# Optimization experiments

Hardware: AMD Instinct MI355X
Metric: run time of the kernel (lower is better)

Reference implementation:

```python
import jax, jax.numpy as jnp
import numpy as np

B, T, C, HR = 8, 4096, 256, 4
N_LAYER, LAYER_ID = 12, 3
HID = HR * C


def _fancy_decay_first():
    # Faithful reproduction of VRWKV_SpatialMix._init_weights(init_mode='fancy')
    r01 = LAYER_ID / (N_LAYER - 1)
    h = np.arange(C, dtype=np.float32)
    decay = -5.0 + 8.0 * (h / (C - 1)) ** (0.7 + 1.3 * r01)
    zig = ((np.arange(1, C + 1) % 3) - 1).astype(np.float32) * 0.5
    first = np.float32(np.log(0.3)) + zig
    return jnp.asarray(decay, jnp.float32), jnp.asarray(first, jnp.float32)


def setup_inputs() -> dict:
    key = jax.random.key(0)
    ks = jax.random.split(key, 12)
    s = 0.02  # small weight scale keeps exp(k) well-conditioned
    decay, first = _fancy_decay_first()
    return {
        "x": jax.random.normal(ks[0], (B, T, C), jnp.float32),
        "Wk": jax.random.normal(ks[1], (C, C), jnp.float32) * s,
        "Wv": jax.random.normal(ks[2], (C, C), jnp.float32) * s,
        "Wr": jax.random.normal(ks[3], (C, C), jnp.float32) * s,
        "Wo": jax.random.normal(ks[4], (C, C), jnp.float32) * s,
        "Wk_ffn": jax.random.normal(ks[5], (C, HID), jnp.float32) * s,
        "Wv_ffn": jax.random.normal(ks[6], (HID, C), jnp.float32) * s,
        "Wr_ffn": jax.random.normal(ks[7], (C, C), jnp.float32) * s,
        "g1": 1.0 + 0.1 * jax.random.normal(ks[8], (C,), jnp.float32),
        "b1": 0.1 * jax.random.normal(ks[9], (C,), jnp.float32),
        "g2": 1.0 + 0.1 * jax.random.normal(ks[10], (C,), jnp.float32),
        "b2": 0.1 * jax.random.normal(ks[11], (C,), jnp.float32),
        "spatial_decay": decay,
        "spatial_first": first,
    }


def _ln(x, g, b):
    m = jnp.mean(x, axis=-1, keepdims=True)
    v = jnp.var(x, axis=-1, keepdims=True)
    return (x - m) * jax.lax.rsqrt(v + 1e-5) * g + b


def _wkv(w, u, k, v):
    # Numerically-stable log-space WKV recurrence (same math as wkv_cuda):
    # y_t = (sum_{i<t} e^{w*(t-1-i)+k_i} v_i + e^{u+k_t} v_t)
    #     / (sum_{i<t} e^{w*(t-1-i)+k_i}     + e^{u+k_t})
    # w,u: [C]; k,v: [B,T,C] -> y: [B,T,C]
    Bb, Tt, Cc = k.shape
    kT = jnp.swapaxes(k, 0, 1)  # [T,B,C]
    vT = jnp.swapaxes(v, 0, 1)

    def step(carry, kv):
        p, q, o = carry           # [B,C] num / den / running max exponent
        kt, vt = kv               # [B,C]
        no = jnp.maximum(o, u + kt)
        A = jnp.exp(o - no)
        E = jnp.exp(u + kt - no)
        y = (A * p + E * vt) / (A * q + E)
        no2 = jnp.maximum(w + o, kt)
        A2 = jnp.exp(w + o - no2)
        E2 = jnp.exp(kt - no2)
        return (A2 * p + E2 * vt, A2 * q + E2, no2), y

    init = (jnp.zeros((Bb, Cc), k.dtype),
            jnp.zeros((Bb, Cc), k.dtype),
            jnp.full((Bb, Cc), -1e38, k.dtype))
    _, yT = jax.lax.scan(step, init, (kT, vT))
    return jnp.swapaxes(yT, 0, 1)


def reference(x, Wk, Wv, Wr, Wo, Wk_ffn, Wv_ffn, Wr_ffn, g1, b1, g2, b2,
              spatial_decay, spatial_first):
    Tlen = x.shape[1]
    # --- SpatialMix (shift_pixel=0 -> xk=xv=xr=h, key_norm=False) ---
    h = _ln(x, g1, b1)
    k = h @ Wk
    v = h @ Wv
    sr = jax.nn.sigmoid(h @ Wr)
    y = _wkv(spatial_decay / Tlen, spatial_first / Tlen, k, v)
    x = x + (sr * y) @ Wo
    # --- ChannelMix (square-ReLU MLP, sigmoid receptance gate) ---
    h2 = _ln(x, g2, b2)
    kk = jnp.square(jax.nn.relu(h2 @ Wk_ffn))
    x = x + jax.nn.sigmoid(h2 @ Wr_ffn) * (kk @ Wv_ffn)
    return x
```

## Files before the change

kernel.cpp:

```cpp
#include <hip/hip_runtime.h>
#include <hip/hip_bf16.h>
#include <math.h>

#define TDIM 4096
#define CDIM 256
#define BDIM 8
#define NTOK (BDIM * TDIM)
#define HIDDIM 1024
#define NCHUNK 128
#define CHLEN 32

typedef float f32x4 __attribute__((ext_vector_type(4)));
typedef __bf16 bf16x8 __attribute__((ext_vector_type(8)));
typedef __bf16 bf16x4 __attribute__((ext_vector_type(4)));

#define GLDS16(gp, lp) __builtin_amdgcn_global_load_lds( \
    (const __attribute__((address_space(1))) void*)(gp), \
    (__attribute__((address_space(3))) void*)(lp), 16, 0, 0)

#define WAITCNT_VM6  0x0F76
#define WAITCNT_VM4  0x0F74
#define WAITCNT_VM2  0x0F72
#define WAITCNT_VM0  0x0F70
#define WAITCNT_VM20 0x4F74

__device__ __forceinline__ float sigm(float v) { return 1.0f / (1.0f + __expf(-v)); }

__global__ __launch_bounds__(256) void pack_weights(
    const float* __restrict__ Wk, const float* __restrict__ Wv,
    const float* __restrict__ Wr, const float* __restrict__ Wo,
    const float* __restrict__ Wkf, const float* __restrict__ Wvf,
    const float* __restrict__ Wrf,
    __bf16* __restrict__ WkvrT, __bf16* __restrict__ WoT,
    __bf16* __restrict__ Wkfr, unsigned char* __restrict__ Wvf8) {
  long long j = (long long)blockIdx.x * 256 + threadIdx.x;
  if (j < 196608) {
    int n = (int)(j >> 8), k = (int)(j & 255);
    const float* src = (n < 256) ? Wk : (n < 512 ? Wv : Wr);
    WkvrT[j] = (__bf16)src[k * 256 + (n & 255)];
    return;
  }
  j -= 196608;
  if (j < 65536) { int n = (int)(j >> 8), k = (int)(j & 255);
    WoT[j] = (__bf16)Wo[k * 256 + n]; return; }
  j -= 65536;
  if (j < 327680) { int n = (int)(j >> 8), k = (int)(j & 255);
    Wkfr[j] = (__bf16)(n < 1024 ? Wkf[(long long)k * 1024 + n]
                                : Wrf[k * 256 + (n - 1024)]);
    return; }
  j -= 327680;
  if (j < 65536) {
    const long long d = j * 4;
    const int n = (int)(d >> 10), k0 = (int)(d & 1023);
    int w = 0;
    w = __builtin_amdgcn_cvt_pk_fp8_f32(Wvf[(long long)k0 * 256 + n],
                                        Wvf[(long long)(k0 + 1) * 256 + n], w, false);
    w = __builtin_amdgcn_cvt_pk_fp8_f32(Wvf[(long long)(k0 + 2) * 256 + n],
                                        Wvf[(long long)(k0 + 3) * 256 + n], w, true);
    *(int*)&Wvf8[d] = w;
    return;
  }
}

__global__ __launch_bounds__(256) void ln_kernel(
    const float* __restrict__ x, const float* __restrict__ gamma,
    const float* __restrict__ beta, __bf16* __restrict__ h) {
  const int wave = threadIdx.x >> 6, lane = threadIdx.x & 63;
  const long long row = (long long)blockIdx.x * 4 + wave;
  const long long base = row * CDIM + lane * 4;
  const f32x4 v = *(const f32x4*)&x[base];
  float s = v[0] + v[1] + v[2] + v[3];
  float s2 = v[0]*v[0] + v[1]*v[1] + v[2]*v[2] + v[3]*v[3];
  #pragma unroll
  for (int o = 1; o < 64; o <<= 1) { s += __shfl_xor(s, o); s2 += __shfl_xor(s2, o); }
  const float mean = s * (1.0f / CDIM);
  const float var = s2 * (1.0f / CDIM) - mean * mean;
  const float rstd = rsqrtf(var + 1e-5f);
  const f32x4 g4 = *(const f32x4*)&gamma[lane * 4];
  const f32x4 b4 = *(const f32x4*)&beta[lane * 4];
  bf16x4 o;
  #pragma unroll
  for (int r = 0; r < 4; r++) o[r] = (__bf16)((v[r] - mean) * rstd * g4[r] + b4[r]);
  *(bf16x4*)&h[base] = o;
}

template <int BN, int EPI, int MT>
__global__ __launch_bounds__(256, 3) void gemm3(
    const __bf16* __restrict__ A, const __bf16* __restrict__ Bt,
    int M, int N,
    __bf16* __restrict__ outH, __bf16* __restrict__ outH2,
    unsigned char* __restrict__ outC,
    const float* __restrict__ srcF,
    const float* __restrict__ gammaP, const float* __restrict__ betaP) {
  constexpr int K = 256;
  constexpr int WNT = BN / 32;
  constexpr int NBC = BN / 64;
  __shared__ __bf16 sA[3][128 * 32];
  __shared__ __bf16 sB[3][BN * 32];
  __shared__ float redS[2][128], redQ[2][128];

  const int tid = threadIdx.x;
  const int wave = tid >> 6, lane = tid & 63;
  const int quad = lane >> 4, mrow = lane & 15;
  const long long bm = (long long)blockIdx.x * (128 * MT);
  const long long bn = (long long)blockIdx.y * BN;
  const int wm = (wave & 1) * 64, wn = (wave >> 1) * (BN / 2);

  const int lrow = lane >> 2;
  const int lk = (lane & 3) * 8;

  auto issue = [&](int g) {
    const int buf = g % 3;
    const long long k0 = (long long)(g & 7) * 32;
    const long long ar = bm + (long long)(g >> 3) * 128;
    const int a0 = wave * 32;
    GLDS16(A + (ar + a0 + lrow) * (long long)K + k0 + lk, &sA[buf][a0 * 32]);
    GLDS16(A + (ar + a0 + 16 + lrow) * (long long)K + k0 + lk, &sA[buf][(a0 + 16) * 32]);
    #pragma unroll
    for (int bc = 0; bc < NBC; bc++) {
      const int r0 = wave * (BN / 4) + bc * 16;
      GLDS16(Bt + (bn + r0 + lrow) * (long long)K + k0 + lk, &sB[buf][r0 * 32]);
    }
  };

  f32x4 acc[4][WNT] = {};

  auto compute = [&](int g) {
    const int buf = g % 3;
    bf16x8 fa[4], fb[WNT];
    #pragma unroll
    for (int mt = 0; mt < 4; mt++)
      fa[mt] = *(const bf16x8*)&sA[buf][(wm + mt * 16 + mrow) * 32 + quad * 8];
    #pragma unroll
    for (int nt = 0; nt < WNT; nt++)
      fb[nt] = *(const bf16x8*)&sB[buf][(wn + nt * 16 + mrow) * 32 + quad * 8];
    #pragma unroll
    for (int mt = 0; mt < 4; mt++)
      #pragma unroll
      for (int nt = 0; nt < WNT; nt++)
        acc[mt][nt] = __builtin_amdgcn_mfma_f32_16x16x32_bf16(fb[nt], fa[mt], acc[mt][nt], 0, 0, 0);
  };

  auto epilogue = [&](int mti) {
    const long long rb0 = bm + (long long)mti * 128;
    #pragma unroll
    for (int mt = 0; mt < 4; mt++) {
      #pragma unroll
      for (int nt = 0; nt < WNT; nt++) {
        const long long row = rb0 + wm + mt * 16 + mrow;
        const int cloc = wn + nt * 16 + quad * 4;
        const long long colb = bn + cloc;
        const f32x4 a = acc[mt][nt];
        if (EPI == 0) {
          const int plane = blockIdx.y >> 1;
          __bf16* o = outH + (long long)plane * ((long long)M * 256);
          const long long c2 = colb & 255;
          bf16x4 v;
          if (plane == 2) {
            #pragma unroll
            for (int r = 0; r < 4; r++) v[r] = (__bf16)sigm(a[r]);
          } else {
            #pragma unroll
            for (int r = 0; r < 4; r++) v[r] = (__bf16)a[r];
          }
          *(bf16x4*)&o[row * 256 + c2] = v;
        } else if (EPI == 2) {
          if (blockIdx.y < 8) {
            float t0 = a[0] > 0.0f ? a[0] : 0.0f;
            float t1 = a[1] > 0.0f ? a[1] : 0.0f;
            float t2 = a[2] > 0.0f ? a[2] : 0.0f;
            float t3 = a[3] > 0.0f ? a[3] : 0.0f;
            int w = 0;
            w = __builtin_amdgcn_cvt_pk_fp8_f32(t0 * t0, t1 * t1, w, false);
            w = __builtin_amdgcn_cvt_pk_fp8_f32(t2 * t2, t3 * t3, w, true);
            *(int*)&outC[row * 1024 + colb] = w;
          } else {
            bf16x4 v;
            #pragma unroll
            for (int r = 0; r < 4; r++) v[r] = (__bf16)sigm(a[r]);
            *(bf16x4*)&outH2[row * 256 + (colb - 1024)] = v;
          }
        }
        acc[mt][nt] = (f32x4){0.0f, 0.0f, 0.0f, 0.0f};
      }
    }
  };

  constexpr int total = 8 * MT;
  issue(0);
  issue(1);

  #pragma unroll 1
  for (int g = 0; g < total; g++) {
    if (g == total - 1)
      __builtin_amdgcn_s_waitcnt(WAITCNT_VM0);
    else if (MT > 1 && g >= 8 && (g & 7) <= 1)
      __builtin_amdgcn_s_waitcnt(WAITCNT_VM20);
    else
      __builtin_amdgcn_s_waitcnt(BN == 256 ? WAITCNT_VM6 : WAITCNT_VM4);
    __builtin_amdgcn_s_barrier();
    if (g + 2 < total) issue(g + 2);
    compute(g);
    if (EPI != 1 && (g & 7) == 7) epilogue(g >> 3);
  }

  if (EPI == 1) {
    float sum[4] = {0, 0, 0, 0}, sq[4] = {0, 0, 0, 0};
    #pragma unroll
    for (int mt = 0; mt < 4; mt++) {
      #pragma unroll
      for (int nt = 0; nt < WNT; nt++) {
        const long long row = bm + wm + mt * 16 + mrow;
        const long long colb = wn + nt * 16 + quad * 4;
        acc[mt][nt] += *(const f32x4*)&srcF[row * 256 + colb];
        #pragma unroll
        for (int r = 0; r < 4; r++) {
          sum[mt] += acc[mt][nt][r];
          sq[mt] += acc[mt][nt][r] * acc[mt][nt][r];
        }
      }
    }
    #pragma unroll
    for (int mt = 0; mt < 4; mt++) {
      sum[mt] += __shfl_xor(sum[mt], 16); sq[mt] += __shfl_xor(sq[mt], 16);
      sum[mt] += __shfl_xor(sum[mt], 32); sq[mt] += __shfl_xor(sq[mt], 32);
    }
    const int wnh = wave >> 1;
    if (quad == 0) {
      #pragma unroll
      for (int mt = 0; mt < 4; mt++) {
        redS[wnh][wm + mt * 16 + mrow] = sum[mt];
        redQ[wnh][wm + mt * 16 + mrow] = sq[mt];
      }
    }
    __syncthreads();
    #pragma unroll
    for (int mt = 0; mt < 4; mt++) {
      const int rb = wm + mt * 16 + mrow;
      const float ts = redS[0][rb] + redS[1][rb];
      const float tq = redQ[0][rb] + redQ[1][rb];
      const float mean = ts * (1.0f / 256.0f);
      const float rstd = rsqrtf(tq * (1.0f / 256.0f) - mean * mean + 1e-5f);
      const long long row = bm + rb;
      #pragma unroll
      for (int nt = 0; nt < WNT; nt++) {
        const long long colb = wn + nt * 16 + quad * 4;
        const f32x4 g4 = *(const f32x4*)&gammaP[colb];
        const f32x4 b4 = *(const f32x4*)&betaP[colb];
        bf16x4 xo, ho;
        #pragma unroll
        for (int r = 0; r < 4; r++) {
          const float t = acc[mt][nt][r];
          xo[r] = (__bf16)t;
          ho[r] = (__bf16)((t - mean) * rstd * g4[r] + b4[r]);
        }
        *(bf16x4*)&outH[row * 256 + colb] = xo;
        *(bf16x4*)&outH2[row * 256 + colb] = ho;
      }
    }
  }
}

__global__ __launch_bounds__(256, 4) void gemm6(
    const unsigned char* __restrict__ A8, const unsigned char* __restrict__ B8,
    float* __restrict__ outF, const __bf16* __restrict__ srcH,
    const __bf16* __restrict__ gate) {
  __shared__ unsigned char sA[3][128 * 32];
  __shared__ unsigned char sB[3][128 * 32];
  const int tid = threadIdx.x;
  const int wave = tid >> 6, lane = tid & 63;
  const int quad = lane >> 4, mrow = lane & 15;
  const long long bm = (long long)blockIdx.x * 128;
  const long long bn = (long long)blockIdx.y * 128;
  const int wm = (wave & 1) * 64, wn = (wave >> 1) * 64;
  const int srow = lane >> 1;
  const int hs = (lane & 1) ^ ((lane >> 2) & 1);

  auto issue = [&](int g) {
    const int buf = g % 3;
    const long long k0 = (long long)g * 32;
    const int a0 = wave * 32;
    GLDS16(A8 + (bm + a0 + srow) * 1024LL + k0 + hs * 16, &sA[buf][a0 * 32]);
    GLDS16(B8 + (bn + a0 + srow) * 1024LL + k0 + hs * 16, &sB[buf][a0 * 32]);
  };

  f32x4 acc[4][4] = {};
  issue(0);
  issue(1);
  const int sw = (mrow >> 1) & 1;

  auto compute = [&](int i) {
    const int buf = i % 3;
    long long fa[4], fb[4];
    const int off = ((((quad >> 1) ^ sw) << 4) | ((quad & 1) << 3));
    #pragma unroll
    for (int mt = 0; mt < 4; mt++)
      fa[mt] = *(const long long*)&sA[buf][(wm + mt * 16 + mrow) * 32 + off];
    #pragma unroll
    for (int nt = 0; nt < 4; nt++)
      fb[nt] = *(const long long*)&sB[buf][(wn + nt * 16 + mrow) * 32 + off];
    #pragma unroll
    for (int mt = 0; mt < 4; mt++)
      #pragma unroll
      for (int nt = 0; nt < 4; nt++)
        acc[mt][nt] = __builtin_amdgcn_mfma_f32_16x16x32_fp8_fp8(fb[nt], fa[mt], acc[mt][nt], 0, 0, 0);
  };

  #pragma unroll 1
  for (int i = 0; i < 31; i++) {
    __builtin_amdgcn_s_waitcnt(WAITCNT_VM2);
    __builtin_amdgcn_s_barrier();
    if (i + 2 < 32) issue(i + 2);
    compute(i);
  }
  __builtin_amdgcn_s_waitcnt(WAITCNT_VM0);
  __builtin_amdgcn_s_barrier();
  compute(31);

  #pragma unroll
  for (int mt = 0; mt < 4; mt++) {
    #pragma unroll
    for (int nt = 0; nt < 4; nt++) {
      const long long row = bm + wm + mt * 16 + mrow;
      const long long colb = bn + wn + nt * 16 + quad * 4;
      const long long idx = row * 256 + colb;
      const f32x4 a = acc[mt][nt];
      const bf16x4 s4 = *(const bf16x4*)&srcH[idx];
      const bf16x4 g4 = *(const bf16x4*)&gate[idx];
      f32x4 v;
      #pragma unroll
      for (int r = 0; r < 4; r++) v[r] = (float)s4[r] + (float)g4[r] * a[r];
      *(f32x4*)&outF[idx] = v;
    }
  }
}

__global__ __launch_bounds__(256) void wkv_phase1(
    const __bf16* __restrict__ ka, const __bf16* __restrict__ va,
    const float* __restrict__ decay,
    float* __restrict__ Sloc, float* __restrict__ Zloc) {
  const int wave = threadIdx.x >> 6, lane = threadIdx.x & 63;
  const int gi = blockIdx.x * 4 + wave;
  const int b = gi >> 7, chunk = gi & (NCHUNK - 1);
  const int c0 = lane * 4;
  const f32x4 w4 = *(const f32x4*)&decay[c0];
  f32x4 ew;
  #pragma unroll
  for (int r = 0; r < 4; r++) ew[r] = __expf(w4[r] * (1.0f / TDIM));
  f32x4 S = {0,0,0,0}, Z = {0,0,0,0};
  long long base = ((long long)b * TDIM + (long long)chunk * CHLEN) * 256 + c0;
  #pragma unroll 4
  for (int t = 0; t < CHLEN; t++) {
    const bf16x4 k4 = *(const bf16x4*)&ka[base + (long long)t * 256];
    const bf16x4 v4 = *(const bf16x4*)&va[base + (long long)t * 256];
    #pragma unroll
    for (int r = 0; r < 4; r++) {
      const float ek = __expf((float)k4[r]);
      S[r] = ew[r] * S[r] + ek * (float)v4[r];
      Z[r] = ew[r] * Z[r] + ek;
    }
  }
  const long long o = (long long)gi * 256 + c0;
  *(f32x4*)&Sloc[o] = S;
  *(f32x4*)&Zloc[o] = Z;
}

__global__ __launch_bounds__(256) void wkv_phase2(
    const float* __restrict__ Sloc, const float* __restrict__ Zloc,
    const float* __restrict__ decay,
    float* __restrict__ Sstart, float* __restrict__ Zstart) {
  const int idx = blockIdx.x * 256 + threadIdx.x;
  const int c = idx & 255;
  const int b = idx >> 8;
  const float w = decay[c] * (1.0f / TDIM);
  const float ewL = __expf(w * (float)CHLEN);
  float S = 0.0f, Z = 0.0f;
  for (int j = 0; j < NCHUNK; j++) {
    const long long o = ((long long)b * NCHUNK + j) * 256 + c;
    Sstart[o] = S;
    Zstart[o] = Z;
    S = ewL * S + Sloc[o];
    Z = ewL * Z + Zloc[o];
  }
}

__global__ __launch_bounds__(256) void wkv_phase3(
    const __bf16* __restrict__ ka, const __bf16* __restrict__ va,
    const __bf16* __restrict__ ra,
    const float* __restrict__ decay, const float* __restrict__ first,
    const float* __restrict__ Sstart, const float* __restrict__ Zstart,
    __bf16* __restrict__ a2) {
  const int wave = threadIdx.x >> 6, lane = threadIdx.x & 63;
  const int gi = blockIdx.x * 4 + wave;
  const int b = gi >> 7, chunk = gi & (NCHUNK - 1);
  const int c0 = lane * 4;
  const f32x4 w4 = *(const f32x4*)&decay[c0];
  const f32x4 u4 = *(const f32x4*)&first[c0];
  f32x4 ew, eu;
  #pragma unroll
  for (int r = 0; r < 4; r++) {
    ew[r] = __expf(w4[r] * (1.0f / TDIM));
    eu[r] = __expf(u4[r] * (1.0f / TDIM));
  }
  const long long so = (long long)gi * 256 + c0;
  f32x4 S = *(const f32x4*)&Sstart[so];
  f32x4 Z = *(const f32x4*)&Zstart[so];
  long long base = ((long long)b * TDIM + (long long)chunk * CHLEN) * 256 + c0;
  #pragma unroll 2
  for (int t = 0; t < CHLEN; t++) {
    const long long p = base + (long long)t * 256;
    const bf16x4 k4 = *(const bf16x4*)&ka[p];
    const bf16x4 v4 = *(const bf16x4*)&va[p];
    const bf16x4 r4 = *(const bf16x4*)&ra[p];
    bf16x4 o;
    #pragma unroll
    for (int r = 0; r < 4; r++) {
      const float ek = __expf((float)k4[r]);
      const float E = eu[r] * ek;
      const float y = (S[r] + E * (float)v4[r]) / (Z[r] + E);
      o[r] = (__bf16)((float)r4[r] * y);
      S[r] = ew[r] * S[r] + ek * (float)v4[r];
      Z[r] = ew[r] * Z[r] + ek;
    }
    *(bf16x4*)&a2[p] = o;
  }
}

extern "C" void kernel_launch(void* const* d_in, const int* in_sizes, int n_in,
                              void* d_out, int out_size, void* d_ws, size_t ws_size,
                              hipStream_t stream) {
  const float* x     = (const float*)d_in[0];
  const float* Wk    = (const float*)d_in[1];
  const float* Wv    = (const float*)d_in[2];
  const float* Wr    = (const float*)d_in[3];
  const float* Wo    = (const float*)d_in[4];
  const float* Wkf   = (const float*)d_in[5];
  const float* Wvf   = (const float*)d_in[6];
  const float* Wrf   = (const float*)d_in[7];
  const float* g1    = (const float*)d_in[8];
  const float* b1    = (const float*)d_in[9];
  const float* g2    = (const float*)d_in[10];
  const float* b2    = (const float*)d_in[11];
  const float* decay = (const float*)d_in[12];
  const float* first = (const float*)d_in[13];
  float* out = (float*)d_out;
  char* ws = (char*)d_ws;

  __bf16* ka     = (__bf16*)(ws + 0);
  __bf16* va     = (__bf16*)(ws + 16777216LL);
  __bf16* ra     = (__bf16*)(ws + 33554432LL);
  __bf16* a2     = (__bf16*)(ws + 50331648LL);
  __bf16* g2buf  = (__bf16*)(ws + 50331648LL);
  __bf16* hbuf   = (__bf16*)(ws + 67108864LL);
  __bf16* h2     = (__bf16*)(ws + 67108864LL);
  __bf16* x1h    = (__bf16*)(ws + 83886080LL);
  float*  Sloc   = (float*)(ws + 100663296LL);
  float*  Zloc   = (float*)(ws + 101711872LL);
  float*  Sstart = (float*)(ws + 102760448LL);
  float*  Zstart = (float*)(ws + 103809024LL);
  unsigned char* kk8 = (unsigned char*)(ws + 100663296LL);
  __bf16* WkvrT  = (__bf16*)(ws + 167772160LL);
  __bf16* WoT    = (__bf16*)(ws + 168165376LL);
  __bf16* Wkfr   = (__bf16*)(ws + 168296448LL);
  unsigned char* Wvf8 = (unsigned char*)(ws + 168951808LL);

  pack_weights<<<2560, 256, 0, stream>>>(Wk, Wv, Wr, Wo, Wkf, Wvf, Wrf,
                                         WkvrT, WoT, Wkfr, Wvf8);

  ln_kernel<<<NTOK / 4, 256, 0, stream>>>(x, g1, b1, hbuf);
  gemm3<128, 0, 2><<<dim3(NTOK / 256, 6), 256, 0, stream>>>(
      hbuf, WkvrT, NTOK, 768, ka, nullptr, nullptr, nullptr, nullptr, nullptr);
  wkv_phase1<<<BDIM * NCHUNK / 4, 256, 0, stream>>>(ka, va, decay, Sloc, Zloc);
  wkv_phase2<<<BDIM, 256, 0, stream>>>(Sloc, Zloc, decay, Sstart, Zstart);
  wkv_phase3<<<BDIM * NCHUNK / 4, 256, 0, stream>>>(ka, va, ra, decay, first,
                                                    Sstart, Zstart, a2);
  gemm3<256, 1, 1><<<dim3(NTOK / 128, 1), 256, 0, stream>>>(
      a2, WoT, NTOK, 256, x1h, h2, nullptr, x, g2, b2);

  gemm3<128, 2, 4><<<dim3(NTOK / 512, 10), 256, 0, stream>>>(
      h2, Wkfr, NTOK, 1280, nullptr, g2buf, kk8, nullptr, nullptr, nullptr);
  gemm6<<<dim3(NTOK / 128, 2), 256, 0, stream>>>(
      kk8, Wvf8, out, x1h, g2buf);
}
```

Before: 287.4 us.

## Split WKV into smaller chunks, add dedicated Wo+LN GEMM, retile FFN GEMM

Doubles the number of WKV chunks while halving their length, so phase 1 and phase 3 launch more waves and each wave runs a shorter serial scan. The Wo projection with its residual add and LayerNorm moves out of gemm3 into a new gemm7 kernel that uses 64-row tiles across the full 256-wide N, giving more blocks and a 4-wave row reduction. The FFN key GEMM now processes 2 M-tiles per block instead of 4, which also doubles its grid. In exchange, the phase-2 serial prefix over chunks becomes twice as long, and the Sloc/Zloc/Sstart/Zstart scratch buffers are relocated to make room for the larger state.

```diff
diff --git a/kernel.cpp b/kernel.cpp
--- a/kernel.cpp
+++ b/kernel.cpp
@@ -7,8 +7,8 @@
 #define BDIM 8
 #define NTOK (BDIM * TDIM)
 #define HIDDIM 1024
-#define NCHUNK 128
-#define CHLEN 32
+#define NCHUNK 256
+#define CHLEN 16
 
 typedef float f32x4 __attribute__((ext_vector_type(4)));
 typedef __bf16 bf16x8 __attribute__((ext_vector_type(8)));
@@ -19,6 +19,7 @@
     (__attribute__((address_space(3))) void*)(lp), 16, 0, 0)
 
 #define WAITCNT_VM6  0x0F76
+#define WAITCNT_VM5  0x0F75
 #define WAITCNT_VM4  0x0F74
 #define WAITCNT_VM2  0x0F72
 #define WAITCNT_VM0  0x0F70
@@ -89,15 +90,12 @@
     const __bf16* __restrict__ A, const __bf16* __restrict__ Bt,
     int M, int N,
     __bf16* __restrict__ outH, __bf16* __restrict__ outH2,
-    unsigned char* __restrict__ outC,
-    const float* __restrict__ srcF,
-    const float* __restrict__ gammaP, const float* __restrict__ betaP) {
+    unsigned char* __restrict__ outC) {
   constexpr int K = 256;
   constexpr int WNT = BN / 32;
   constexpr int NBC = BN / 64;
   __shared__ __bf16 sA[3][128 * 32];
   __shared__ __bf16 sB[3][BN * 32];
-  __shared__ float redS[2][128], redQ[2][128];
 
   const int tid = threadIdx.x;
   const int wave = tid >> 6, lane = tid & 63;
@@ -192,71 +190,134 @@
 
   #pragma unroll 1
   for (int g = 0; g < total; g++) {
-    if (g == total - 1)
+    if (g == total - 1) {
       __builtin_amdgcn_s_waitcnt(WAITCNT_VM0);
-    else if (MT > 1 && g >= 8 && (g & 7) <= 1)
+    } else if (MT > 1 && g >= 8 && (g & 7) <= 1) {
       __builtin_amdgcn_s_waitcnt(WAITCNT_VM20);
-    else
-      __builtin_amdgcn_s_waitcnt(BN == 256 ? WAITCNT_VM6 : WAITCNT_VM4);
+    } else if (BN == 256) {
+      __builtin_amdgcn_s_waitcnt(WAITCNT_VM6);
+    } else {
+      __builtin_amdgcn_s_waitcnt(WAITCNT_VM4);
+    }
     __builtin_amdgcn_s_barrier();
     if (g + 2 < total) issue(g + 2);
     compute(g);
-    if (EPI != 1 && (g & 7) == 7) epilogue(g >> 3);
-  }
-
-  if (EPI == 1) {
-    float sum[4] = {0, 0, 0, 0}, sq[4] = {0, 0, 0, 0};
+    if ((g & 7) == 7) epilogue(g >> 3);
+  }
+}
+
+__global__ __launch_bounds__(256, 2) void gemm7(
+    const __bf16* __restrict__ A, const __bf16* __restrict__ Bt,
+    const float* __restrict__ x,
+    const float* __restrict__ gammaP, const float* __restrict__ betaP,
+    __bf16* __restrict__ x1h, __bf16* __restrict__ h2) {
+  constexpr int K = 256;
+  __shared__ __bf16 sA[3][64 * 32];
+  __shared__ __bf16 sB[3][256 * 32];
+  __shared__ float redS[4][64], redQ[4][64];
+
+  const int tid = threadIdx.x;
+  const int wave = tid >> 6, lane = tid & 63;
+  const int quad = lane >> 4, mrow = lane & 15;
+  const long long bm = (long long)blockIdx.x * 64;
+  const int wn = wave * 64;
+  const int lrow = lane >> 2;
+  const int lk = (lane & 3) * 8;
+
+  auto issue = [&](int g) {
+    const int buf = g % 3;
+    const long long k0 = (long long)g * 32;
+    GLDS16(A + (bm + wave * 16 + lrow) * (long long)K + k0 + lk,
+           &sA[buf][(wave * 16) * 32]);
+    #pragma unroll
+    for (int bc = 0; bc < 4; bc++) {
+      const int r0 = wave * 64 + bc * 16;
+      GLDS16(Bt + (r0 + lrow) * (long long)K + k0 + lk, &sB[buf][r0 * 32]);
+    }
+  };
+
+  f32x4 acc[4][4] = {};
+
+  auto compute = [&](int g) {
+    const int buf = g % 3;
+    bf16x8 fa[4], fb[4];
+    #pragma unroll
+    for (int mt = 0; mt < 4; mt++)
+      fa[mt] = *(const bf16x8*)&sA[buf][(mt * 16 + mrow) * 32 + quad * 8];
+    #pragma unroll
+    for (int nt = 0; nt < 4; nt++)
+      fb[nt] = *(const bf16x8*)&sB[buf][(wn + nt * 16 + mrow) * 32 + quad * 8];
+    #pragma unroll
+    for (int mt = 0; mt < 4; mt++)
+      #pragma unroll
+      for (int nt = 0; nt < 4; nt++)
+        acc[mt][nt] = __builtin_amdgcn_mfma_f32_16x16x32_bf16(fb[nt], fa[mt], acc[mt][nt], 0, 0, 0);
+  };
+
+  issue(0);
+  issue(1);
+  #pragma unroll 1
+  for (int g = 0; g < 8; g++) {
+    if (g == 7) {
+      __builtin_amdgcn_s_waitcnt(WAITCNT_VM0);
+    } else {
+      __builtin_amdgcn_s_waitcnt(WAITCNT_VM5);
+    }
+    __builtin_amdgcn_s_barrier();
+    if (g + 2 < 8) issue(g + 2);
+    compute(g);
+  }
+
+  float sum[4] = {0, 0, 0, 0}, sq[4] = {0, 0, 0, 0};
+  #pragma unroll
+  for (int mt = 0; mt < 4; mt++) {
+    #pragma unroll
+    for (int nt = 0; nt < 4; nt++) {
+      const long long row = bm + mt * 16 + mrow;
+      const long long colb = wn + nt * 16 + quad * 4;
+      acc[mt][nt] += *(const f32x4*)&x[row * 256 + colb];
+      #pragma unroll
+      for (int r = 0; r < 4; r++) {
+        sum[mt] += acc[mt][nt][r];
+        sq[mt] += acc[mt][nt][r] * acc[mt][nt][r];
+      }
+    }
+  }
+  #pragma unroll
+  for (int mt = 0; mt < 4; mt++) {
+    sum[mt] += __shfl_xor(sum[mt], 16); sq[mt] += __shfl_xor(sq[mt], 16);
+    sum[mt] += __shfl_xor(sum[mt], 32); sq[mt] += __shfl_xor(sq[mt], 32);
+  }
+  if (quad == 0) {
     #pragma unroll
     for (int mt = 0; mt < 4; mt++) {
-      #pragma unroll
-      for (int nt = 0; nt < WNT; nt++) {
-        const long long row = bm + wm + mt * 16 + mrow;
-        const long long colb = wn + nt * 16 + quad * 4;
-        acc[mt][nt] += *(const f32x4*)&srcF[row * 256 + colb];
-        #pragma unroll
-        for (int r = 0; r < 4; r++) {
-          sum[mt] += acc[mt][nt][r];
-          sq[mt] += acc[mt][nt][r] * acc[mt][nt][r];
-        }
+      redS[wave][mt * 16 + mrow] = sum[mt];
+      redQ[wave][mt * 16 + mrow] = sq[mt];
+    }
+  }
+  __syncthreads();
+  #pragma unroll
+  for (int mt = 0; mt < 4; mt++) {
+    const int rb = mt * 16 + mrow;
+    const float ts = redS[0][rb] + redS[1][rb] + redS[2][rb] + redS[3][rb];
+    const float tq = redQ[0][rb] + redQ[1][rb] + redQ[2][rb] + redQ[3][rb];
+    const float mean = ts * (1.0f / 256.0f);
+    const float rstd = rsqrtf(tq * (1.0f / 256.0f) - mean * mean + 1e-5f);
+    const long long row = bm + rb;
+    #pragma unroll
+    for (int nt = 0; nt < 4; nt++) {
+      const long long colb = wn + nt * 16 + quad * 4;
+      const f32x4 g4 = *(const f32x4*)&gammaP[colb];
+      const f32x4 b4 = *(const f32x4*)&betaP[colb];
+      bf16x4 xo, ho;
+      #pragma unroll
+      for (int r = 0; r < 4; r++) {
+        const float t = acc[mt][nt][r];
+        xo[r] = (__bf16)t;
+        ho[r] = (__bf16)((t - mean) * rstd * g4[r] + b4[r]);
       }
-    }
-    #pragma unroll
-    for (int mt = 0; mt < 4; mt++) {
-      sum[mt] += __shfl_xor(sum[mt], 16); sq[mt] += __shfl_xor(sq[mt], 16);
-      sum[mt] += __shfl_xor(sum[mt], 32); sq[mt] += __shfl_xor(sq[mt], 32);
-    }
-    const int wnh = wave >> 1;
-    if (quad == 0) {
-      #pragma unroll
-      for (int mt = 0; mt < 4; mt++) {
-        redS[wnh][wm + mt * 16 + mrow] = sum[mt];
-        redQ[wnh][wm + mt * 16 + mrow] = sq[mt];
-      }
-    }
-    __syncthreads();
-    #pragma unroll
-    for (int mt = 0; mt < 4; mt++) {
-      const int rb = wm + mt * 16 + mrow;
-      const float ts = redS[0][rb] + redS[1][rb];
-      const float tq = redQ[0][rb] + redQ[1][rb];
-      const float mean = ts * (1.0f / 256.0f);
-      const float rstd = rsqrtf(tq * (1.0f / 256.0f) - mean * mean + 1e-5f);
-      const long long row = bm + rb;
-      #pragma unroll
-      for (int nt = 0; nt < WNT; nt++) {
-        const long long colb = wn + nt * 16 + quad * 4;
-        const f32x4 g4 = *(const f32x4*)&gammaP[colb];
-        const f32x4 b4 = *(const f32x4*)&betaP[colb];
-        bf16x4 xo, ho;
-        #pragma unroll
-        for (int r = 0; r < 4; r++) {
-          const float t = acc[mt][nt][r];
-          xo[r] = (__bf16)t;
-          ho[r] = (__bf16)((t - mean) * rstd * g4[r] + b4[r]);
-        }
-        *(bf16x4*)&outH[row * 256 + colb] = xo;
-        *(bf16x4*)&outH2[row * 256 + colb] = ho;
-      }
+      *(bf16x4*)&x1h[row * 256 + colb] = xo;
+      *(bf16x4*)&h2[row * 256 + colb] = ho;
     }
   }
 }
@@ -341,7 +402,7 @@
     float* __restrict__ Sloc, float* __restrict__ Zloc) {
   const int wave = threadIdx.x >> 6, lane = threadIdx.x & 63;
   const int gi = blockIdx.x * 4 + wave;
-  const int b = gi >> 7, chunk = gi & (NCHUNK - 1);
+  const int b = gi >> 8, chunk = gi & (NCHUNK - 1);
   const int c0 = lane * 4;
   const f32x4 w4 = *(const f32x4*)&decay[c0];
   f32x4 ew;
@@ -392,7 +453,7 @@
     __bf16* __restrict__ a2) {
   const int wave = threadIdx.x >> 6, lane = threadIdx.x & 63;
   const int gi = blockIdx.x * 4 + wave;
-  const int b = gi >> 7, chunk = gi & (NCHUNK - 1);
+  const int b = gi >> 8, chunk = gi & (NCHUNK - 1);
   const int c0 = lane * 4;
   const f32x4 w4 = *(const f32x4*)&decay[c0];
   const f32x4 u4 = *(const f32x4*)&first[c0];
@@ -454,11 +515,11 @@
   __bf16* hbuf   = (__bf16*)(ws + 67108864LL);
   __bf16* h2     = (__bf16*)(ws + 67108864LL);
   __bf16* x1h    = (__bf16*)(ws + 83886080LL);
-  float*  Sloc   = (float*)(ws + 100663296LL);
-  float*  Zloc   = (float*)(ws + 101711872LL);
-  float*  Sstart = (float*)(ws + 102760448LL);
-  float*  Zstart = (float*)(ws + 103809024LL);
   unsigned char* kk8 = (unsigned char*)(ws + 100663296LL);
+  float*  Sloc   = (float*)(ws + 134217728LL);
+  float*  Zloc   = (float*)(ws + 137363456LL);
+  float*  Sstart = (float*)(ws + 140509184LL);
+  float*  Zstart = (float*)(ws + 143654912LL);
   __bf16* WkvrT  = (__bf16*)(ws + 167772160LL);
   __bf16* WoT    = (__bf16*)(ws + 168165376LL);
   __bf16* Wkfr   = (__bf16*)(ws + 168296448LL);
@@ -469,16 +530,15 @@
 
   ln_kernel<<<NTOK / 4, 256, 0, stream>>>(x, g1, b1, hbuf);
   gemm3<128, 0, 2><<<dim3(NTOK / 256, 6), 256, 0, stream>>>(
-      hbuf, WkvrT, NTOK, 768, ka, nullptr, nullptr, nullptr, nullptr, nullptr);
+      hbuf, WkvrT, NTOK, 768, ka, nullptr, nullptr);
   wkv_phase1<<<BDIM * NCHUNK / 4, 256, 0, stream>>>(ka, va, decay, Sloc, Zloc);
   wkv_phase2<<<BDIM, 256, 0, stream>>>(Sloc, Zloc, decay, Sstart, Zstart);
   wkv_phase3<<<BDIM * NCHUNK / 4, 256, 0, stream>>>(ka, va, ra, decay, first,
                                                     Sstart, Zstart, a2);
-  gemm3<256, 1, 1><<<dim3(NTOK / 128, 1), 256, 0, stream>>>(
-      a2, WoT, NTOK, 256, x1h, h2, nullptr, x, g2, b2);
-
-  gemm3<128, 2, 4><<<dim3(NTOK / 512, 10), 256, 0, stream>>>(
-      h2, Wkfr, NTOK, 1280, nullptr, g2buf, kk8, nullptr, nullptr, nullptr);
+  gemm7<<<NTOK / 64, 256, 0, stream>>>(a2, WoT, x, g2, b2, x1h, h2);
+
+  gemm3<128, 2, 2><<<dim3(NTOK / 256, 10), 256, 0, stream>>>(
+      h2, Wkfr, NTOK, 1280, nullptr, g2buf, kk8);
   gemm6<<<dim3(NTOK / 128, 2), 256, 0, stream>>>(
       kk8, Wvf8, out, x1h, g2buf);
 }
```

Measured after the change: 279.1 us. -2.9%, faster.
